# Optimization experiments

Hardware: AMD Instinct MI355X
Metric: run time of the kernel (lower is better)

The kernel has to match this reference:

```python
import jax, jax.numpy as jnp
import numpy as np

TOP_K = 2


def setup_inputs() -> dict:
    key = jax.random.key(0)
    k0, k1, k2, k3, k4 = jax.random.split(key, 5)
    B, S, D, F, E = 4, 2048, 2048, 1408, 8
    scale = 0.02
    return {
        "hidden_states": jax.random.normal(k0, (B, S, D), jnp.float32),
        "router_w": jax.random.normal(k1, (D, E), jnp.float32) * scale,
        "w_gate": jax.random.normal(k2, (E, D, F), jnp.float32) * scale,
        "w_up": jax.random.normal(k3, (E, D, F), jnp.float32) * scale,
        "w_down": jax.random.normal(k4, (E, F, D), jnp.float32) * scale,
    }


def reference(hidden_states, router_w, w_gate, w_up, w_down):
    B, S, D = hidden_states.shape
    x = hidden_states.reshape(-1, D)              # [N, D]
    N = x.shape[0]
    E = router_w.shape[-1]

    # ---- Router: softmax over experts, top-k, renormalize top-k probs ----
    logits = x @ router_w                         # [N, E]
    probs = jax.nn.softmax(logits, axis=-1)
    top_w, top_i = jax.lax.top_k(probs, TOP_K)    # [N, K]
    top_w = top_w / jnp.sum(top_w, axis=-1, keepdims=True)

    # Dense gate matrix [N, E]: gate is the (renormalized) routing weight for
    # selected experts, zero otherwise.
    gates = jnp.zeros_like(probs).at[jnp.arange(N)[:, None], top_i].set(top_w)

    # ---- Load-balancing aux loss (Switch-style, averaged over top-k) ----
    f = jnp.mean(jnp.sum(jax.nn.one_hot(top_i, E, dtype=x.dtype), axis=1), axis=0)  # [E] dispatch fraction
    P = jnp.mean(probs, axis=0)                   # [E] mean router prob
    aux_loss = (E / TOP_K) * jnp.sum(f * P)

    # ---- Per-expert SwiGLU FFN, computed as grouped GEMMs over all experts ----
    g = jnp.einsum("nd,edf->enf", x, w_gate)      # [E, N, F]
    u = jnp.einsum("nd,edf->enf", x, w_up)        # [E, N, F]
    h = jax.nn.silu(g) * u                        # [E, N, F]
    expert_out = jnp.einsum("enf,efd->end", h, w_down)  # [E, N, D]

    # ---- Combine: gate-weighted sum over experts ----
    out = jnp.einsum("ne,end->nd", gates, expert_out)   # [N, D]
    return out.reshape(B, S, D), aux_loss
```

## Files before the change

kernel.cpp:

```cpp
#include <hip/hip_runtime.h>

#define N_TOK 8192
#define DIM   2048
#define FFN   1408

#define XB_OFF  0ull
#define HP_OFF  0ull
#define XGP_OFF 49020928ull
#define EO_OFF  49020928ull
#define P1_OFF  120324096ull
#define P2_OFF  212598784ull
#define LPK_OFF 258736128ull
#define TI_OFF  258801664ull
#define TW_OFF  258834432ull
#define TP_OFF  258867200ull
#define ST_OFF  258932736ull

typedef __bf16 bf16x8 __attribute__((ext_vector_type(8)));
typedef float  f32x4  __attribute__((ext_vector_type(4)));
typedef int    int4v  __attribute__((ext_vector_type(4)));
typedef __attribute__((address_space(1))) void as1_void;
typedef __attribute__((address_space(3))) void as3_void;

__device__ __forceinline__ void gload16(const void* g, void* l) {
  __builtin_amdgcn_global_load_lds((as1_void*)g, (as3_void*)l, 16, 0, 0);
}

__device__ __forceinline__ ushort f2bf(float f) {
  unsigned u = __builtin_bit_cast(unsigned, f);
  u += 0x7FFFu + ((u >> 16) & 1u);
  return (ushort)(u >> 16);
}
__device__ __forceinline__ float blo(unsigned w) { return __builtin_bit_cast(float, w << 16); }
__device__ __forceinline__ float bhi(unsigned w) { return __builtin_bit_cast(float, w & 0xffff0000u); }

__device__ __forceinline__ int4v dsread(int addr) {
  int4v d;
  asm volatile("ds_read_b128 %0, %1" : "=v"(d) : "v"(addr));
  return d;
}

#define BAR()   __builtin_amdgcn_s_barrier()
#define MFMA16(a, b, c) __builtin_amdgcn_mfma_f32_16x16x32_bf16(a, b, c, 0, 0, 0)
#define BC(x) __builtin_bit_cast(bf16x8, x)

__device__ __forceinline__ int swz(int row, int s) {
  int q = row >> 1;
  int p = (((row & 1) << 2) | s) ^ (q & 7);
  return q * 128 + p * 16;
}

__global__ __launch_bounds__(256) void prep_kernel(
    const float* __restrict__ x, const float* __restrict__ rw,
    ushort* __restrict__ xb, int* __restrict__ topi, float* __restrict__ topw,
    int* __restrict__ cnt, unsigned long long* __restrict__ psum,
    const float* __restrict__ wg, const float* __restrict__ wu,
    const float* __restrict__ wd, char* __restrict__ p1, char* __restrict__ p2)
{
  __shared__ char smem[16640];
  int b = blockIdx.x;

  if (b < 512) {
    int tid = threadIdx.x, lane = tid & 63, wv = tid >> 6;
    float (*sP)[8] = (float(*)[8])smem;
    int   (*sC)[8] = (int(*)[8])(smem + 128);
    float pacc[8]; int cacc[8];
    #pragma unroll
    for (int e = 0; e < 8; ++e) { pacc[e] = 0.f; cacc[e] = 0; }

    #pragma unroll 1
    for (int it = 0; it < 4; ++it) {
      int t = b * 16 + wv * 4 + it;
      const float4* xr = (const float4*)(x + (size_t)t * DIM);
      float acc[8];
      #pragma unroll
      for (int e = 0; e < 8; ++e) acc[e] = 0.f;
      #pragma unroll 1
      for (int i = 0; i < 8; ++i) {
        int j = i * 64 + lane;
        float4 v = xr[j];
        ushort4 o; o.x = f2bf(v.x); o.y = f2bf(v.y); o.z = f2bf(v.z); o.w = f2bf(v.w);
        *(ushort4*)(xb + (size_t)t * DIM + (size_t)j * 4) = o;
        const float* rr = rw + (size_t)j * 32;
        #pragma unroll
        for (int c = 0; c < 4; ++c) {
          float xv = (&v.x)[c];
          const float4* r4 = (const float4*)(rr + c * 8);
          float4 q0 = r4[0], q1 = r4[1];
          acc[0] += xv * q0.x; acc[1] += xv * q0.y; acc[2] += xv * q0.z; acc[3] += xv * q0.w;
          acc[4] += xv * q1.x; acc[5] += xv * q1.y; acc[6] += xv * q1.z; acc[7] += xv * q1.w;
        }
      }
      #pragma unroll
      for (int off = 32; off; off >>= 1) {
        #pragma unroll
        for (int e = 0; e < 8; ++e) acc[e] += __shfl_xor(acc[e], off);
      }
      float m = acc[0];
      #pragma unroll
      for (int e = 1; e < 8; ++e) m = fmaxf(m, acc[e]);
      float p[8], s = 0.f;
      #pragma unroll
      for (int e = 0; e < 8; ++e) { p[e] = __expf(acc[e] - m); s += p[e]; }
      float inv = 1.f / s;
      int i1 = 0; float p1v = p[0];
      #pragma unroll
      for (int e = 1; e < 8; ++e) if (p[e] > p1v) { p1v = p[e]; i1 = e; }
      int i2 = -1; float p2v = -1.f;
      #pragma unroll
      for (int e = 0; e < 8; ++e) if (e != i1 && p[e] > p2v) { p2v = p[e]; i2 = e; }
      float w1 = p1v / (p1v + p2v);
      if (lane == 0) {
        topi[t] = i1 | (i2 << 8);
        topw[t] = w1;
        #pragma unroll
        for (int e = 0; e < 8; ++e) pacc[e] += p[e] * inv;
        cacc[i1]++; cacc[i2]++;
      }
    }
    if (lane == 0) {
      #pragma unroll
      for (int e = 0; e < 8; ++e) { sP[wv][e] = pacc[e]; sC[wv][e] = cacc[e]; }
    }
    __syncthreads();
    if (tid < 8) {
      float ps = sP[0][tid] + sP[1][tid] + sP[2][tid] + sP[3][tid];
      int   cs = sC[0][tid] + sC[1][tid] + sC[2][tid] + sC[3][tid];
      atomicAdd(&cnt[tid], cs);
      atomicAdd(&psum[tid], (unsigned long long)((double)ps * 1099511627776.0));
    }
  } else if (b < 11776) {
    int q_ = b - 512;
    int j = q_ & 63, rest = q_ >> 6;
    int tn = rest % 22, e = rest / 22;
    float (*tg)[65] = (float(*)[65])smem;
    float (*tu)[65] = (float(*)[65])(smem + 8320);
    int t = threadIdx.x;
    const float* gs = wg + ((size_t)e * DIM + j * 32) * FFN + tn * 64;
    const float* us = wu + ((size_t)e * DIM + j * 32) * FFN + tn * 64;
    #pragma unroll
    for (int k2 = 0; k2 < 2; ++k2) {
      int idx = t + k2 * 256;
      int kk = idx >> 4, fq = idx & 15;
      *(float4*)&tg[kk][fq * 4] = *(const float4*)(gs + (size_t)kk * FFN + fq * 4);
      *(float4*)&tu[kk][fq * 4] = *(const float4*)(us + (size_t)kk * FFN + fq * 4);
    }
    __syncthreads();
    char* dst = p1 + ((size_t)((e * 22 + tn) * 64 + j)) * 8192;
    #pragma unroll
    for (int k2 = 0; k2 < 2; ++k2) {
      int L = t + k2 * 256;
      int q = L >> 3, v = (L & 7) ^ (q & 7);
      int r = 2 * q + (v >> 2), s = v & 3;
      const float* col = (r < 64) ? &tg[s * 8][r] : &tu[s * 8][r - 64];
      ushort u8[8];
      #pragma unroll
      for (int i = 0; i < 8; ++i) u8[i] = f2bf(col[i * 65]);
      *(ushort4*)(dst + (size_t)L * 16) = *(ushort4*)&u8[0];
      *(ushort4*)(dst + (size_t)L * 16 + 8) = *(ushort4*)&u8[4];
    }
  } else {
    int q_ = b - 11776;
    int j = q_ % 44, rest = q_ / 44;
    int tn = rest & 15, e = rest >> 4;
    float (*t2)[129] = (float(*)[129])smem;
    int t = threadIdx.x;
    const float* src = wd + ((size_t)e * FFN + j * 32) * DIM + tn * 128;
    #pragma unroll
    for (int k2 = 0; k2 < 4; ++k2) {
      int idx = t + k2 * 256;
      int kk = idx >> 5, dq = idx & 31;
      *(float4*)&t2[kk][dq * 4] = *(const float4*)(src + (size_t)kk * DIM + dq * 4);
    }
    __syncthreads();
    char* dst = p2 + ((size_t)((e * 16 + tn) * 44 + j)) * 8192;
    #pragma unroll
    for (int k2 = 0; k2 < 2; ++k2) {
      int L = t + k2 * 256;
      int q = L >> 3, v = (L & 7) ^ (q & 7);
      int r = 2 * q + (v >> 2), s = v & 3;
      ushort u8[8];
      #pragma unroll
      for (int i = 0; i < 8; ++i) u8[i] = f2bf(t2[s * 8 + i][r]);
      *(ushort4*)(dst + (size_t)L * 16) = *(ushort4*)&u8[0];
      *(ushort4*)(dst + (size_t)L * 16 + 8) = *(ushort4*)&u8[4];
    }
  }
}

__global__ __launch_bounds__(256) void place_kernel(
    const int* __restrict__ topi, int* __restrict__ stats,
    const unsigned long long* __restrict__ psum,
    int* __restrict__ lpk, int2* __restrict__ tpos, float* __restrict__ aux_out)
{
  int cnt[8], pre[8];
  int acc = 0;
  #pragma unroll
  for (int e = 0; e < 8; ++e) { cnt[e] = stats[e]; pre[e] = acc; acc += cnt[e]; }

  if (blockIdx.x == 0 && threadIdx.x == 0) {
    int tb = 0;
    for (int e = 0; e < 8; ++e) {
      stats[16 + e] = pre[e];
      stats[24 + e] = tb;
      tb += (cnt[e] + 127) >> 7;
    }
    stats[32] = tb;
    double s = 0.0;
    for (int e = 0; e < 8; ++e)
      s += (double)cnt[e] * ((double)psum[e] * (1.0 / 1099511627776.0));
    aux_out[0] = (float)(4.0 * s / ((double)N_TOK * (double)N_TOK));
  }

  int t = blockIdx.x * 256 + threadIdx.x;
  if (t >= N_TOK) return;
  int pk = topi[t];
  int e1 = pk & 0xff, e2 = (pk >> 8) & 0xff;
  int p1 = pre[e1] + atomicAdd(&stats[8 + e1], 1);
  lpk[p1] = t;
  int p2 = pre[e2] + atomicAdd(&stats[8 + e2], 1);
  lpk[p2] = t;
  tpos[t] = make_int2(p1, p2);
}

__global__ __launch_bounds__(256) void gather_x_kernel(
    const ushort* __restrict__ xb, const int* __restrict__ lpk,
    const int* __restrict__ stats, char* __restrict__ xgp)
{
  int b = blockIdx.x;
  int tile = b >> 2;
  if (tile >= stats[32]) return;
  int e = 0;
  #pragma unroll
  for (int k = 1; k < 8; ++k) if (tile >= stats[24 + k]) e = k;
  int tloc = tile - stats[24 + e];
  int abase = stats[16 + e], Me = stats[e];
  int quad = b & 3;
  int lane = threadIdx.x & 63, wv = threadIdx.x >> 6;
  char* base = xgp + (size_t)tile * 64 * 8192;
  #pragma unroll 1
  for (int r = quad * 32 + wv; r < quad * 32 + 32; r += 4) {
    int lrow = tloc * 128 + r;
    bool valid = lrow < Me;
    const char* src = (const char*)xb + (valid ? (size_t)lpk[abase + lrow] * (DIM * 2) : 0);
    int q = r >> 1;
    #pragma unroll
    for (int it = 0; it < 4; ++it) {
      int c16 = it * 64 + lane;
      int j = c16 >> 2, s = c16 & 3;
      uint4 v;
      if (valid) v = *(const uint4*)(src + c16 * 16);
      else       v = make_uint4(0, 0, 0, 0);
      int p = (((r & 1) << 2) | s) ^ (q & 7);
      *(uint4*)(base + (size_t)j * 8192 + q * 128 + p * 16) = v;
    }
  }
}


#define GSTAGE(J, BUF) do { \
  size_t go_ = (size_t)(J) * 8192 + wv * 2048 + lane * 16; \
  int d_ = (BUF) * 24576 + wv * 2048; \
  gload16(aP0 + go_,        sm + d_); \
  gload16(aP0 + go_ + 1024, sm + d_ + 1024); \
  gload16(aP1 + go_,        sm + d_ + 8192); \
  gload16(aP1 + go_ + 1024, sm + d_ + 8192 + 1024); \
  gload16(bP + go_,         sm + d_ + 16384); \
  gload16(bP + go_ + 1024,  sm + d_ + 16384 + 1024); \
} while (0)

#define KLOOP(NCH) \
  GSTAGE(0, 0); \
  GSTAGE(1, 1); \
  { int cur = 0, st = 2; \
  _Pragma("unroll 1") \
  for (int j = 0; j < (NCH); ++j) { \
    if (j + 2 < (NCH)) { \
      GSTAGE(j + 2, st); \
      asm volatile("s_waitcnt vmcnt(12)" ::: "memory"); \
    } else if (j + 2 == (NCH)) { \
      asm volatile("s_waitcnt vmcnt(6)" ::: "memory"); \
    } else { \
      asm volatile("s_waitcnt vmcnt(0)" ::: "memory"); \
    } \
    BAR(); \
    int sb = cur * 24576; \
    int4v va[4], vb[8]; \
    _Pragma("unroll") for (int n = 0; n < 4; ++n) vb[n] = dsread(sb + adB[n]); \
    _Pragma("unroll") for (int m = 0; m < 4; ++m) va[m] = dsread(sb + adA[m]); \
    _Pragma("unroll") for (int n = 4; n < 8; ++n) vb[n] = dsread(sb + adB[n]); \
    asm volatile("s_waitcnt lgkmcnt(4)" ::: "memory"); \
    __builtin_amdgcn_sched_barrier(0); \
    __builtin_amdgcn_s_setprio(1); \
    _Pragma("unroll") for (int m = 0; m < 4; ++m) \
      _Pragma("unroll") for (int n = 0; n < 4; ++n) \
        acc[m][n] = MFMA16(BC(va[m]), BC(vb[n]), acc[m][n]); \
    __builtin_amdgcn_s_setprio(0); \
    asm volatile("s_waitcnt lgkmcnt(0)" ::: "memory"); \
    __builtin_amdgcn_sched_barrier(0); \
    __builtin_amdgcn_s_setprio(1); \
    _Pragma("unroll") for (int m = 0; m < 4; ++m) \
      _Pragma("unroll") for (int n = 4; n < 8; ++n) \
        acc[m][n] = MFMA16(BC(va[m]), BC(vb[n]), acc[m][n]); \
    __builtin_amdgcn_s_setprio(0); \
    BAR(); \
    cur = (cur == 2) ? 0 : cur + 1; \
    st  = (st  == 2) ? 0 : st  + 1; \
  } }

__global__ __launch_bounds__(256, 2) void gemm_gu_kernel(
    const char* __restrict__ xgp, const char* __restrict__ p1,
    const int* __restrict__ stats, char* __restrict__ hp)
{
  int bid = blockIdx.x;
  int e = bid & 7;
  int Ll = bid >> 3;
  int tm = Ll / 22, tn = Ll % 22;
  int Me = stats[e];
  if (tm * 256 >= Me) return;
  int tb = stats[24 + e];

  __shared__ char sm[73728];
  int tid = threadIdx.x, lane = tid & 63, wv = tid >> 6;
  const char* aP0 = xgp + (size_t)(tb + tm * 2) * 64 * 8192;
  const char* aP1 = aP0 + 64 * 8192;
  const char* bP = p1 + (size_t)((e * 22 + tn) * 64) * 8192;

  int s = lane >> 4;
  int adA[4], adB[8];
  #pragma unroll
  for (int m = 0; m < 4; ++m) {
    int row = wv * 64 + m * 16 + (lane & 15);
    adA[m] = (row >> 7) * 8192 + swz(row & 127, s);
  }
  #pragma unroll
  for (int n = 0; n < 8; ++n) adB[n] = 16384 + swz(n * 16 + (lane & 15), s);

  f32x4 acc[4][8];
  #pragma unroll
  for (int m = 0; m < 4; ++m)
    #pragma unroll
    for (int n = 0; n < 8; ++n) acc[m][n] = (f32x4){0, 0, 0, 0};

  KLOOP(64);

  int r0 = (lane >> 4) * 4, cl = lane & 15;
  #pragma unroll
  for (int m = 0; m < 4; ++m) {
    #pragma unroll
    for (int r = 0; r < 4; ++r) {
      int row = wv * 64 + m * 16 + r0 + r;
      if (tm * 256 + row < Me) {
        char* hb = hp + (size_t)(tb + tm * 2 + (row >> 7)) * 44 * 8192;
        int lr = row & 127;
        int q = lr >> 1;
        #pragma unroll
        for (int n = 0; n < 4; ++n) {
          float g = acc[m][n][r];
          float u = acc[m][n + 4][r];
          float hv = g * u / (1.f + __expf(-g));
          int f = tn * 64 + n * 16 + cl;
          int j2 = f >> 5, s2 = (f >> 3) & 3, i2 = f & 7;
          int p = (((lr & 1) << 2) | s2) ^ (q & 7);
          *(ushort*)(hb + (size_t)j2 * 8192 + q * 128 + p * 16 + i2 * 2) = f2bf(hv);
        }
      }
    }
  }
}

__global__ __launch_bounds__(256, 2) void gemm_down_kernel(
    const char* __restrict__ hp, const char* __restrict__ p2,
    const int* __restrict__ stats, ushort* __restrict__ eo)
{
  int bid = blockIdx.x;
  int e = bid & 7;
  int Ll = bid >> 3;
  int tm = Ll >> 4, tn = Ll & 15;
  int Me = stats[e];
  if (tm * 256 >= Me) return;
  int tb = stats[24 + e], abase = stats[16 + e];

  __shared__ char sm[73728];
  int tid = threadIdx.x, lane = tid & 63, wv = tid >> 6;
  const char* aP0 = hp + (size_t)(tb + tm * 2) * 44 * 8192;
  const char* aP1 = aP0 + 44 * 8192;
  const char* bP = p2 + (size_t)((e * 16 + tn) * 44) * 8192;

  int s = lane >> 4;
  int adA[4], adB[8];
  #pragma unroll
  for (int m = 0; m < 4; ++m) {
    int row = wv * 64 + m * 16 + (lane & 15);
    adA[m] = (row >> 7) * 8192 + swz(row & 127, s);
  }
  #pragma unroll
  for (int n = 0; n < 8; ++n) adB[n] = 16384 + swz(n * 16 + (lane & 15), s);

  f32x4 acc[4][8];
  #pragma unroll
  for (int m = 0; m < 4; ++m)
    #pragma unroll
    for (int n = 0; n < 8; ++n) acc[m][n] = (f32x4){0, 0, 0, 0};

  KLOOP(44);

  int c0 = lane & 15, r0 = (lane >> 4) * 4;
  #pragma unroll
  for (int m = 0; m < 4; ++m) {
    #pragma unroll
    for (int r = 0; r < 4; ++r) {
      int lrow = tm * 256 + wv * 64 + m * 16 + r0 + r;
      if (lrow < Me) {
        ushort* dst = eo + (size_t)(abase + lrow) * DIM + tn * 128 + c0;
        #pragma unroll
        for (int n = 0; n < 8; ++n) dst[n * 16] = f2bf(acc[m][n][r]);
      }
    }
  }
}

__global__ __launch_bounds__(256) void combine_kernel(
    const ushort* __restrict__ eo, const int2* __restrict__ tpos,
    const float* __restrict__ topw, float* __restrict__ out)
{
  int t = blockIdx.x;
  int2 tp = tpos[t];
  float w1 = topw[t], w2 = 1.f - w1;
  const uint4* r1 = (const uint4*)(eo + (size_t)tp.x * DIM);
  const uint4* r2 = (const uint4*)(eo + (size_t)tp.y * DIM);
  float4* o = (float4*)(out + (size_t)t * DIM);
  int i = threadIdx.x;
  uint4 a = r1[i], b = r2[i];
  float4 c0, c1;
  c0.x = w1 * blo(a.x) + w2 * blo(b.x);  c0.y = w1 * bhi(a.x) + w2 * bhi(b.x);
  c0.z = w1 * blo(a.y) + w2 * blo(b.y);  c0.w = w1 * bhi(a.y) + w2 * bhi(b.y);
  c1.x = w1 * blo(a.z) + w2 * blo(b.z);  c1.y = w1 * bhi(a.z) + w2 * bhi(b.z);
  c1.z = w1 * blo(a.w) + w2 * blo(b.w);  c1.w = w1 * bhi(a.w) + w2 * bhi(b.w);
  o[i * 2] = c0;
  o[i * 2 + 1] = c1;
}

extern "C" void kernel_launch(void* const* d_in, const int* in_sizes, int n_in,
                              void* d_out, int out_size, void* d_ws, size_t ws_size,
                              hipStream_t stream)
{
  const float* x  = (const float*)d_in[0];
  const float* rw = (const float*)d_in[1];
  const float* wg = (const float*)d_in[2];
  const float* wu = (const float*)d_in[3];
  const float* wd = (const float*)d_in[4];
  float* out = (float*)d_out;

  char* ws = (char*)d_ws;
  ushort* xb   = (ushort*)(ws + XB_OFF);
  char*   hp   = ws + HP_OFF;
  char*   xgp  = ws + XGP_OFF;
  ushort* eo   = (ushort*)(ws + EO_OFF);
  char*   p1   = ws + P1_OFF;
  char*   p2   = ws + P2_OFF;
  int*    lpk  = (int*)(ws + LPK_OFF);
  int*    topi = (int*)(ws + TI_OFF);
  float*  topw = (float*)(ws + TW_OFF);
  int2*   tpos = (int2*)(ws + TP_OFF);
  int*    stats = (int*)(ws + ST_OFF);
  unsigned long long* psum = (unsigned long long*)(ws + ST_OFF + 192);

  hipMemsetAsync(ws + ST_OFF, 0, 256, stream);

  prep_kernel<<<17408, 256, 0, stream>>>(x, rw, xb, topi, topw, stats, psum,
                                         wg, wu, wd, p1, p2);
  place_kernel<<<32, 256, 0, stream>>>(topi, stats, psum, lpk, tpos,
                                       out + (size_t)out_size - 1);

  gather_x_kernel<<<544, 256, 0, stream>>>(xb, lpk, stats, xgp);

  gemm_gu_kernel<<<2816, 256, 0, stream>>>(xgp, p1, stats, hp);
  gemm_down_kernel<<<2048, 256, 0, stream>>>(hp, p2, stats, eo);

  combine_kernel<<<8192, 256, 0, stream>>>(eo, tpos, topw, out);
}
```

Before: 517.4 us.

## Use 2-wave blocks with 128x128 warp tiles in expert GEMMs

Both grouped GEMM kernels now run 128-thread blocks in which each wave computes 128 rows by 128 columns, instead of four waves computing 64 rows each. Each wave issues more global-to-LDS loads per stage and more MFMAs per LDS read. The intent is to raise the MFMA-to-LDS-read ratio and cut redundant B-fragment reads across waves. In exchange it doubles accumulator registers (256 VGPRs for acc), forces one block per launch bound, and leaves fewer waves per CU to hide latency.

```diff
diff --git a/kernel.cpp b/kernel.cpp
--- a/kernel.cpp
+++ b/kernel.cpp
@@ -259,14 +259,14 @@
 
 
 #define GSTAGE(J, BUF) do { \
-  size_t go_ = (size_t)(J) * 8192 + wv * 2048 + lane * 16; \
-  int d_ = (BUF) * 24576 + wv * 2048; \
-  gload16(aP0 + go_,        sm + d_); \
-  gload16(aP0 + go_ + 1024, sm + d_ + 1024); \
-  gload16(aP1 + go_,        sm + d_ + 8192); \
-  gload16(aP1 + go_ + 1024, sm + d_ + 8192 + 1024); \
-  gload16(bP + go_,         sm + d_ + 16384); \
-  gload16(bP + go_ + 1024,  sm + d_ + 16384 + 1024); \
+  size_t go_ = (size_t)(J) * 8192 + lane * 16; \
+  const char* aw_ = wv ? aP1 : aP0; \
+  char* db_ = sm + (BUF) * 24576 + wv * 8192; \
+  _Pragma("unroll") for (int i_ = 0; i_ < 8; ++i_) \
+    gload16(aw_ + go_ + i_ * 1024, db_ + i_ * 1024); \
+  char* dbB_ = sm + (BUF) * 24576 + 16384 + wv * 4096; \
+  _Pragma("unroll") for (int i_ = 0; i_ < 4; ++i_) \
+    gload16(bP + go_ + wv * 4096 + i_ * 1024, dbB_ + i_ * 1024); \
 } while (0)
 
 #define KLOOP(NCH) \
@@ -277,29 +277,29 @@
   for (int j = 0; j < (NCH); ++j) { \
     if (j + 2 < (NCH)) { \
       GSTAGE(j + 2, st); \
+      asm volatile("s_waitcnt vmcnt(24)" ::: "memory"); \
+    } else if (j + 2 == (NCH)) { \
       asm volatile("s_waitcnt vmcnt(12)" ::: "memory"); \
-    } else if (j + 2 == (NCH)) { \
-      asm volatile("s_waitcnt vmcnt(6)" ::: "memory"); \
     } else { \
       asm volatile("s_waitcnt vmcnt(0)" ::: "memory"); \
     } \
     BAR(); \
     int sb = cur * 24576; \
-    int4v va[4], vb[8]; \
+    int4v va[8], vb[8]; \
     _Pragma("unroll") for (int n = 0; n < 4; ++n) vb[n] = dsread(sb + adB[n]); \
-    _Pragma("unroll") for (int m = 0; m < 4; ++m) va[m] = dsread(sb + adA[m]); \
+    _Pragma("unroll") for (int m = 0; m < 8; ++m) va[m] = dsread(sb + adA[m]); \
     _Pragma("unroll") for (int n = 4; n < 8; ++n) vb[n] = dsread(sb + adB[n]); \
     asm volatile("s_waitcnt lgkmcnt(4)" ::: "memory"); \
     __builtin_amdgcn_sched_barrier(0); \
     __builtin_amdgcn_s_setprio(1); \
-    _Pragma("unroll") for (int m = 0; m < 4; ++m) \
+    _Pragma("unroll") for (int m = 0; m < 8; ++m) \
       _Pragma("unroll") for (int n = 0; n < 4; ++n) \
         acc[m][n] = MFMA16(BC(va[m]), BC(vb[n]), acc[m][n]); \
     __builtin_amdgcn_s_setprio(0); \
     asm volatile("s_waitcnt lgkmcnt(0)" ::: "memory"); \
     __builtin_amdgcn_sched_barrier(0); \
     __builtin_amdgcn_s_setprio(1); \
-    _Pragma("unroll") for (int m = 0; m < 4; ++m) \
+    _Pragma("unroll") for (int m = 0; m < 8; ++m) \
       _Pragma("unroll") for (int n = 4; n < 8; ++n) \
         acc[m][n] = MFMA16(BC(va[m]), BC(vb[n]), acc[m][n]); \
     __builtin_amdgcn_s_setprio(0); \
@@ -308,7 +308,7 @@
     st  = (st  == 2) ? 0 : st  + 1; \
   } }
 
-__global__ __launch_bounds__(256, 2) void gemm_gu_kernel(
+__global__ __launch_bounds__(128, 1) void gemm_gu_kernel(
     const char* __restrict__ xgp, const char* __restrict__ p1,
     const int* __restrict__ stats, char* __restrict__ hp)
 {
@@ -327,32 +327,28 @@
   const char* bP = p1 + (size_t)((e * 22 + tn) * 64) * 8192;
 
   int s = lane >> 4;
-  int adA[4], adB[8];
-  #pragma unroll
-  for (int m = 0; m < 4; ++m) {
-    int row = wv * 64 + m * 16 + (lane & 15);
-    adA[m] = (row >> 7) * 8192 + swz(row & 127, s);
-  }
+  int adA[8], adB[8];
+  #pragma unroll
+  for (int m = 0; m < 8; ++m) adA[m] = wv * 8192 + swz(m * 16 + (lane & 15), s);
   #pragma unroll
   for (int n = 0; n < 8; ++n) adB[n] = 16384 + swz(n * 16 + (lane & 15), s);
 
-  f32x4 acc[4][8];
-  #pragma unroll
-  for (int m = 0; m < 4; ++m)
+  f32x4 acc[8][8];
+  #pragma unroll
+  for (int m = 0; m < 8; ++m)
     #pragma unroll
     for (int n = 0; n < 8; ++n) acc[m][n] = (f32x4){0, 0, 0, 0};
 
   KLOOP(64);
 
   int r0 = (lane >> 4) * 4, cl = lane & 15;
-  #pragma unroll
-  for (int m = 0; m < 4; ++m) {
+  char* hb = hp + (size_t)(tb + tm * 2 + wv) * 44 * 8192;
+  #pragma unroll
+  for (int m = 0; m < 8; ++m) {
     #pragma unroll
     for (int r = 0; r < 4; ++r) {
-      int row = wv * 64 + m * 16 + r0 + r;
-      if (tm * 256 + row < Me) {
-        char* hb = hp + (size_t)(tb + tm * 2 + (row >> 7)) * 44 * 8192;
-        int lr = row & 127;
+      int lr = m * 16 + r0 + r;
+      if (tm * 256 + wv * 128 + lr < Me) {
         int q = lr >> 1;
         #pragma unroll
         for (int n = 0; n < 4; ++n) {
@@ -369,7 +365,7 @@
   }
 }
 
-__global__ __launch_bounds__(256, 2) void gemm_down_kernel(
+__global__ __launch_bounds__(128, 1) void gemm_down_kernel(
     const char* __restrict__ hp, const char* __restrict__ p2,
     const int* __restrict__ stats, ushort* __restrict__ eo)
 {
@@ -388,18 +384,15 @@
   const char* bP = p2 + (size_t)((e * 16 + tn) * 44) * 8192;
 
   int s = lane >> 4;
-  int adA[4], adB[8];
-  #pragma unroll
-  for (int m = 0; m < 4; ++m) {
-    int row = wv * 64 + m * 16 + (lane & 15);
-    adA[m] = (row >> 7) * 8192 + swz(row & 127, s);
-  }
+  int adA[8], adB[8];
+  #pragma unroll
+  for (int m = 0; m < 8; ++m) adA[m] = wv * 8192 + swz(m * 16 + (lane & 15), s);
   #pragma unroll
   for (int n = 0; n < 8; ++n) adB[n] = 16384 + swz(n * 16 + (lane & 15), s);
 
-  f32x4 acc[4][8];
-  #pragma unroll
-  for (int m = 0; m < 4; ++m)
+  f32x4 acc[8][8];
+  #pragma unroll
+  for (int m = 0; m < 8; ++m)
     #pragma unroll
     for (int n = 0; n < 8; ++n) acc[m][n] = (f32x4){0, 0, 0, 0};
 
@@ -407,10 +400,10 @@
 
   int c0 = lane & 15, r0 = (lane >> 4) * 4;
   #pragma unroll
-  for (int m = 0; m < 4; ++m) {
+  for (int m = 0; m < 8; ++m) {
     #pragma unroll
     for (int r = 0; r < 4; ++r) {
-      int lrow = tm * 256 + wv * 64 + m * 16 + r0 + r;
+      int lrow = tm * 256 + wv * 128 + m * 16 + r0 + r;
       if (lrow < Me) {
         ushort* dst = eo + (size_t)(abase + lrow) * DIM + tn * 128 + c0;
         #pragma unroll
@@ -475,8 +468,8 @@
 
   gather_x_kernel<<<544, 256, 0, stream>>>(xb, lpk, stats, xgp);
 
-  gemm_gu_kernel<<<2816, 256, 0, stream>>>(xgp, p1, stats, hp);
-  gemm_down_kernel<<<2048, 256, 0, stream>>>(hp, p2, stats, eo);
+  gemm_gu_kernel<<<2816, 128, 0, stream>>>(xgp, p1, stats, hp);
+  gemm_down_kernel<<<2048, 128, 0, stream>>>(hp, p2, stats, eo);
 
   combine_kernel<<<8192, 256, 0, stream>>>(eo, tpos, topw, out);
 }
```

Measured after the change: 957.5 us. 85.0% more time.
